# Optimization experiments

Measured on AMD Instinct MI355X. Metric: run time of the kernel, lower is better.

Reference implementation:

```python
import jax, jax.numpy as jnp
import numpy as np

B, S, D = 1, 2048, 4096
H, KVH, DH = 32, 8, 128
NEG_INF = jnp.finfo(jnp.float32).min


def rotate_half(x):
    x1, x2 = jnp.split(x, 2, axis=-1)
    return jnp.concatenate([-x2, x1], axis=-1)


def setup_inputs() -> dict:
    key = jax.random.key(0)
    ks = jax.random.split(key, 6)
    hidden_states = jax.random.normal(ks[0], (B, S, D), dtype=jnp.float32)
    # proper llama RoPE tables
    inv_freq = 1.0 / (10000.0 ** (jnp.arange(0, DH, 2, dtype=jnp.float32) / DH))
    pos = jnp.arange(S, dtype=jnp.float32)
    freqs = pos[:, None] * inv_freq[None, :]            # [S, DH/2]
    emb = jnp.concatenate([freqs, freqs], axis=-1)       # [S, DH]
    cos = jnp.cos(emb)
    sin = jnp.sin(emb)
    # additive causal mask [B,1,S,S]
    causal = jnp.tril(jnp.ones((S, S), dtype=bool))
    attention_mask = jnp.where(causal, 0.0, NEG_INF)[None, None].astype(jnp.float32)
    sc = 0.02
    Wq = jax.random.normal(ks[1], (D, H * DH), dtype=jnp.float32) * sc
    Wk = jax.random.normal(ks[2], (D, KVH * DH), dtype=jnp.float32) * sc
    Wv = jax.random.normal(ks[3], (D, KVH * DH), dtype=jnp.float32) * sc
    Wo = jax.random.normal(ks[4], (H * DH, D), dtype=jnp.float32) * sc
    return {"hidden_states": hidden_states, "cos": cos, "sin": sin,
            "attention_mask": attention_mask, "Wq": Wq, "Wk": Wk, "Wv": Wv, "Wo": Wo}


def reference(hidden_states, cos, sin, attention_mask, Wq, Wk, Wv, Wo):
    b, s, _ = hidden_states.shape
    scaling = DH ** -0.5
    q = (hidden_states @ Wq).reshape(b, s, H, DH).transpose(0, 2, 1, 3)     # [B,H,S,DH]
    k = (hidden_states @ Wk).reshape(b, s, KVH, DH).transpose(0, 2, 1, 3)   # [B,KVH,S,DH]
    v = (hidden_states @ Wv).reshape(b, s, KVH, DH).transpose(0, 2, 1, 3)
    c = cos[None, None]  # [1,1,S,DH]
    sn = sin[None, None]
    q = q * c + rotate_half(q) * sn
    k = k * c + rotate_half(k) * sn
    n_rep = H // KVH
    k = jnp.repeat(k, n_rep, axis=1)  # [B,H,S,DH]
    v = jnp.repeat(v, n_rep, axis=1)
    scores = jnp.einsum('bhqd,bhkd->bhqk', q, k) * scaling
    scores = jnp.maximum(scores + attention_mask, NEG_INF)
    probs = jax.nn.softmax(scores.astype(jnp.float32), axis=-1).astype(q.dtype)
    attn = jnp.einsum('bhqk,bhkd->bhqd', probs, v)
    attn = attn.transpose(0, 2, 1, 3).reshape(b, s, H * DH)
    return attn @ Wo
```

## Files before the change

kernel.cpp:

```cpp
#include <hip/hip_runtime.h>
#include <hip/hip_bf16.h>
#include <stdint.h>

typedef unsigned short u16;
typedef unsigned int u32;
typedef __bf16 bf16x8 __attribute__((ext_vector_type(8)));
typedef float f32x4 __attribute__((ext_vector_type(4)));
typedef u16 u16x8 __attribute__((ext_vector_type(8)));

#define S_LEN 2048
#define DMODEL 4096
#define NHEADS 32
#define NKVH 8
#define DHEAD 128
#define LDQK 6144

__device__ __forceinline__ float bf2f(u16 x) {
    union { u32 i; float f; } u; u.i = ((u32)x) << 16; return u.f;
}
__device__ __forceinline__ u16 f2bf(float f) {
    union { float f; u32 i; } u; u.f = f;
    u32 x = u.i;
    return (u16)((x + 0x7fffu + ((x >> 16) & 1u)) >> 16);
}
__device__ __forceinline__ bf16x8 ld_bf8(const void* p) {
    int4 v = *(const int4*)p;
    return __builtin_bit_cast(bf16x8, v);
}

__global__ void k_cvt(const float* __restrict__ in, u16* __restrict__ out, int n8) {
    int i = blockIdx.x * 256 + threadIdx.x;
    if (i >= n8) return;
    const float4* p = (const float4*)in + (size_t)i * 2;
    float4 a = p[0], b = p[1];
    u16x8 o;
    o[0]=f2bf(a.x); o[1]=f2bf(a.y); o[2]=f2bf(a.z); o[3]=f2bf(a.w);
    o[4]=f2bf(b.x); o[5]=f2bf(b.y); o[6]=f2bf(b.z); o[7]=f2bf(b.w);
    *((u16x8*)out + i) = o;
}

template<typename TIN>
__global__ void k_transpose_bf16(const TIN* __restrict__ in, u16* __restrict__ out,
                                 int R, int C, int ldin) {
    __shared__ u16 tile[32][33];
    int c0 = blockIdx.x * 32, r0 = blockIdx.y * 32;
    int tx = threadIdx.x & 31, ty = threadIdx.x >> 5;
    #pragma unroll
    for (int i = 0; i < 4; i++) {
        int r = ty + i * 8;
        TIN v = in[(size_t)(r0 + r) * ldin + c0 + tx];
        if constexpr (sizeof(TIN) == 4) tile[r][tx] = f2bf((float)v);
        else tile[r][tx] = (u16)v;
    }
    __syncthreads();
    #pragma unroll
    for (int i = 0; i < 4; i++) {
        int r = ty + i * 8;
        out[(size_t)(c0 + r) * R + r0 + tx] = tile[tx][r];
    }
}

__global__ void k_rope(u16* __restrict__ X, const float* __restrict__ cosT,
                       const float* __restrict__ sinT, int nh, int ld) {
    int idx = blockIdx.x * 256 + threadIdx.x;
    int d = idx & 63;
    int h = (idx >> 6) % nh;
    int s = idx / (64 * nh);
    u16* p = X + (size_t)s * ld + h * DHEAD;
    float x1 = bf2f(p[d]), x2 = bf2f(p[d + 64]);
    float c1 = cosT[s * DHEAD + d],      s1 = sinT[s * DHEAD + d];
    float c2 = cosT[s * DHEAD + d + 64], s2 = sinT[s * DHEAD + d + 64];
    p[d]      = f2bf(x1 * c1 - x2 * s1);
    p[d + 64] = f2bf(x2 * c2 + x1 * s2);
}

typedef const __attribute__((address_space(1))) u32 GBUF;
typedef __attribute__((address_space(3))) u32 LBUF;

template<typename OUT_T>
__global__ __launch_bounds__(256)
void k_gemm_bt(const u16* __restrict__ A, const u16* __restrict__ Bt,
               OUT_T* __restrict__ C, int M, int N, int K) {
    __shared__ __align__(16) u16 As[128 * 32];
    __shared__ __align__(16) u16 Bs[128 * 32];
    const int m0 = blockIdx.y * 128, n0 = blockIdx.x * 128;
    const int tid = threadIdx.x, lane = tid & 63, wid = tid >> 6;
    const int wr = wid >> 1, wc = wid & 1;
    const int g = lane >> 4, lr = lane & 15;

    f32x4 acc[4][4] = {};

    for (int k0 = 0; k0 < K; k0 += 32) {
        __syncthreads();
        #pragma unroll
        for (int j = 0; j < 2; j++) {
            int c = wid * 128 + j * 64 + lane;
            int r = c >> 2, co = (c & 3) << 3;
            __builtin_amdgcn_global_load_lds((GBUF*)(A  + (size_t)(m0 + r) * K + k0 + co),
                                             (LBUF*)(As + (size_t)(wid * 128 + j * 64) * 8), 16, 0, 0);
            __builtin_amdgcn_global_load_lds((GBUF*)(Bt + (size_t)(n0 + r) * K + k0 + co),
                                             (LBUF*)(Bs + (size_t)(wid * 128 + j * 64) * 8), 16, 0, 0);
        }
        __syncthreads();
        bf16x8 af[4], bf[4];
        #pragma unroll
        for (int i = 0; i < 4; i++)
            af[i] = ld_bf8(As + (wr * 64 + i * 16 + lr) * 32 + g * 8);
        #pragma unroll
        for (int i = 0; i < 4; i++)
            bf[i] = ld_bf8(Bs + (wc * 64 + i * 16 + lr) * 32 + g * 8);
        #pragma unroll
        for (int i = 0; i < 4; i++)
            #pragma unroll
            for (int n = 0; n < 4; n++)
                acc[i][n] = __builtin_amdgcn_mfma_f32_16x16x32_bf16(af[i], bf[n], acc[i][n], 0, 0, 0);
    }
    #pragma unroll
    for (int i = 0; i < 4; i++)
        #pragma unroll
        for (int n = 0; n < 4; n++)
            #pragma unroll
            for (int r = 0; r < 4; r++) {
                int row = m0 + wr * 64 + i * 16 + g * 4 + r;
                int col = n0 + wc * 64 + n * 16 + lr;
                float v = acc[i][n][r];
                if constexpr (sizeof(OUT_T) == 2) C[(size_t)row * N + col] = f2bf(v);
                else                              C[(size_t)row * N + col] = v;
            }
}

__global__ __launch_bounds__(256)
void k_attn2(const u16* __restrict__ Qb, const u16* __restrict__ Kb,
             const u16* __restrict__ VbT, u16* __restrict__ Ab) {
    extern __shared__ __align__(16) char smem[];

    const int p = blockIdx.x, h = blockIdx.y, hk = h >> 2;
    const int tid = threadIdx.x, lane = tid & 63, wid = tid >> 6;
    const int g = lane >> 4, lr = lane & 15;
    const float scale = 0.08838834764831845f;
    const int qtA = p, qtB = 31 - p, nA = qtA + 1;
    const int NIT = 33;

    const int krow_l = lane >> 4, kc16 = lane & 15;
    const int vrow_l = lane >> 3, vc8  = lane & 7;

    u16* PsB = (u16*)(smem + 65536) + wid * 16 * 72;

    auto stage = [&](int buf, int k0) {
        u16* KsD = (u16*)smem + buf * 8192;
        u16* VtD = (u16*)(smem + 32768) + buf * 8192;
        #pragma unroll
        for (int j = 0; j < 4; j++) {
            int rowt = wid * 16 + j * 4 + krow_l;
            int c16  = kc16 ^ (rowt & 7);
            __builtin_amdgcn_global_load_lds(
                (GBUF*)(Kb + (size_t)(k0 + rowt) * LDQK + hk * DHEAD + c16 * 8),
                (LBUF*)(KsD + (wid * 16 + j * 4) * 128), 16, 0, 0);
        }
        #pragma unroll
        for (int j = 0; j < 4; j++) {
            int rowt = wid * 32 + j * 8 + vrow_l;
            int c8   = vc8 ^ (rowt & 7);
            __builtin_amdgcn_global_load_lds(
                (GBUF*)(VbT + (size_t)(hk * DHEAD + rowt) * S_LEN + k0 + c8 * 8),
                (LBUF*)(VtD + (wid * 32 + j * 8) * 64), 16, 0, 0);
        }
    };

    bf16x8 qf[4];
    f32x4 acc[8];
    float m[4], lsum[4];
    int qt = qtA, q0 = qtA * 64;

    stage(0, 0);
    asm volatile("s_waitcnt vmcnt(0)" ::: "memory");
    __builtin_amdgcn_s_barrier();

    for (int i = 0; i < NIT; i++) {
        const int kt = (i < nA) ? i : (i - nA);
        if (i + 1 < NIT) {
            int kt1 = (i + 1 < nA) ? (i + 1) : (i + 1 - nA);
            stage((i + 1) & 1, kt1 * 64);
        }
        if (i == 0 || i == nA) {
            if (i == nA) {
                #pragma unroll
                for (int n = 0; n < 8; n++)
                    #pragma unroll
                    for (int r = 0; r < 4; r++)
                        Ab[(size_t)(q0 + wid * 16 + g * 4 + r) * DMODEL + h * DHEAD + n * 16 + lr]
                            = f2bf(acc[n][r] / lsum[r]);
            }
            qt = (i == 0) ? qtA : qtB;
            q0 = qt * 64;
            const u16* qrow = Qb + (size_t)(q0 + wid * 16 + lr) * LDQK + h * DHEAD;
            #pragma unroll
            for (int c = 0; c < 4; c++) qf[c] = ld_bf8(qrow + c * 32 + g * 8);
            #pragma unroll
            for (int n = 0; n < 8; n++) acc[n] = (f32x4){0.f, 0.f, 0.f, 0.f};
            #pragma unroll
            for (int r = 0; r < 4; r++) { m[r] = -1e30f; lsum[r] = 0.f; }
        }

        const char* KsB = smem + (i & 1) * 16384;
        const char* VtB = smem + 32768 + (i & 1) * 16384;

        f32x4 sf[4];
        __builtin_amdgcn_s_setprio(1);
        #pragma unroll
        for (int st = 0; st < 4; st++) {
            f32x4 s = {0.f, 0.f, 0.f, 0.f};
            #pragma unroll
            for (int c = 0; c < 4; c++) {
                int row = st * 16 + lr;
                int cb = (c * 32 + g * 8) * 2;
                bf16x8 kf = ld_bf8(KsB + row * 256 + (cb ^ ((row & 7) << 4)));
                s = __builtin_amdgcn_mfma_f32_16x16x32_bf16(qf[c], kf, s, 0, 0, 0);
            }
            sf[st] = s;
        }
        __builtin_amdgcn_s_setprio(0);

        if (kt == qt) {
            #pragma unroll
            for (int st = 0; st < 4; st++)
                #pragma unroll
                for (int r = 0; r < 4; r++) {
                    int qg = wid * 16 + g * 4 + r;
                    int kg = st * 16 + lr;
                    sf[st][r] = (kg > qg) ? -1e30f : sf[st][r] * scale;
                }
        } else {
            #pragma unroll
            for (int st = 0; st < 4; st++)
                #pragma unroll
                for (int r = 0; r < 4; r++) sf[st][r] *= scale;
        }

        float corr[4];
        #pragma unroll
        for (int r = 0; r < 4; r++) {
            float v = fmaxf(fmaxf(sf[0][r], sf[1][r]), fmaxf(sf[2][r], sf[3][r]));
            #pragma unroll
            for (int off = 1; off < 16; off <<= 1) v = fmaxf(v, __shfl_xor(v, off, 64));
            float mn = fmaxf(m[r], v);
            corr[r] = __expf(m[r] - mn);
            m[r] = mn;
        }
        float ts[4] = {0.f, 0.f, 0.f, 0.f};
        #pragma unroll
        for (int st = 0; st < 4; st++)
            #pragma unroll
            for (int r = 0; r < 4; r++) {
                float pv = __expf(sf[st][r] - m[r]);
                sf[st][r] = pv;
                ts[r] += pv;
            }
        #pragma unroll
        for (int r = 0; r < 4; r++) {
            #pragma unroll
            for (int off = 1; off < 16; off <<= 1) ts[r] += __shfl_xor(ts[r], off, 64);
            lsum[r] = lsum[r] * corr[r] + ts[r];
        }
        #pragma unroll
        for (int n = 0; n < 8; n++)
            #pragma unroll
            for (int r = 0; r < 4; r++) acc[n][r] *= corr[r];

        #pragma unroll
        for (int st = 0; st < 4; st++)
            #pragma unroll
            for (int r = 0; r < 4; r++)
                PsB[(g * 4 + r) * 72 + st * 16 + lr] = f2bf(sf[st][r]);
        asm volatile("s_waitcnt lgkmcnt(0)" ::: "memory");

        __builtin_amdgcn_s_setprio(1);
        #pragma unroll
        for (int c2 = 0; c2 < 2; c2++) {
            bf16x8 pa = ld_bf8(PsB + lr * 72 + c2 * 32 + g * 8);
            #pragma unroll
            for (int n = 0; n < 8; n++) {
                int row = n * 16 + lr;
                int cb = (c2 * 32 + g * 8) * 2;
                bf16x8 vf = ld_bf8(VtB + row * 128 + (cb ^ ((row & 7) << 4)));
                acc[n] = __builtin_amdgcn_mfma_f32_16x16x32_bf16(pa, vf, acc[n], 0, 0, 0);
            }
        }
        __builtin_amdgcn_s_setprio(0);

        asm volatile("s_waitcnt lgkmcnt(0)" ::: "memory");
        __builtin_amdgcn_sched_barrier(0);
        asm volatile("s_waitcnt vmcnt(0)" ::: "memory");
        __builtin_amdgcn_s_barrier();
    }

    #pragma unroll
    for (int n = 0; n < 8; n++)
        #pragma unroll
        for (int r = 0; r < 4; r++)
            Ab[(size_t)(q0 + wid * 16 + g * 4 + r) * DMODEL + h * DHEAD + n * 16 + lr]
                = f2bf(acc[n][r] / lsum[r]);
}

extern "C" void kernel_launch(void* const* d_in, const int* in_sizes, int n_in,
                              void* d_out, int out_size, void* d_ws, size_t ws_size,
                              hipStream_t stream) {
    const float* hidden = (const float*)d_in[0];
    const float* cosT   = (const float*)d_in[1];
    const float* sinT   = (const float*)d_in[2];
    const float* Wq = (const float*)d_in[4];
    const float* Wk = (const float*)d_in[5];
    const float* Wv = (const float*)d_in[6];
    const float* Wo = (const float*)d_in[7];
    float* out = (float*)d_out;
    char* ws = (char*)d_ws;

    u16* Xbf   = (u16*)ws;
    u16* WqkvT = (u16*)(ws + (16u << 20));
    u16* VbT   = (u16*)(ws + (16u << 20));
    u16* WoT   = (u16*)(ws + (64u << 20));
    u16* QKVb  = (u16*)(ws + (96u << 20));
    u16* Ab    = Xbf;

    k_cvt<<<dim3((S_LEN * DMODEL / 8) / 256), 256, 0, stream>>>(hidden, Xbf, S_LEN * DMODEL / 8);
    k_transpose_bf16<float><<<dim3(4096 / 32, 4096 / 32), 256, 0, stream>>>(Wq, WqkvT, 4096, 4096, 4096);
    k_transpose_bf16<float><<<dim3(1024 / 32, 4096 / 32), 256, 0, stream>>>(Wk, WqkvT + (size_t)4096 * 4096, 4096, 1024, 1024);
    k_transpose_bf16<float><<<dim3(1024 / 32, 4096 / 32), 256, 0, stream>>>(Wv, WqkvT + (size_t)5120 * 4096, 4096, 1024, 1024);
    k_transpose_bf16<float><<<dim3(4096 / 32, 4096 / 32), 256, 0, stream>>>(Wo, WoT, 4096, 4096, 4096);

    k_gemm_bt<u16><<<dim3(6144 / 128, 2048 / 128), 256, 0, stream>>>(Xbf, WqkvT, QKVb, 2048, 6144, 4096);

    k_rope<<<(2048 * 32 * 64) / 256, 256, 0, stream>>>(QKVb, cosT, sinT, 32, LDQK);
    k_rope<<<(2048 * 8 * 64) / 256, 256, 0, stream>>>(QKVb + 4096, cosT, sinT, 8, LDQK);

    k_transpose_bf16<u16><<<dim3(1024 / 32, 2048 / 32), 256, 0, stream>>>(QKVb + 5120, VbT, 2048, 1024, LDQK);

    hipFuncSetAttribute((const void*)k_attn2, hipFuncAttributeMaxDynamicSharedMemorySize, 74752);
    k_attn2<<<dim3(16, 32), 256, 74752, stream>>>(QKVb, QKVb + 4096, VbT, Ab);

    k_gemm_bt<float><<<dim3(4096 / 128, 2048 / 128), 256, 0, stream>>>(Ab, WoT, out, 2048, 4096, 4096);
}
```

Measured before the change: 411.6 us.

## Replace 128x128 GEMM with pipelined 256x256 tile kernel and split-K output projection

Replaces the simple 128x128-tile GEMM with a 512-thread 256x256-tile kernel. It double-buffers 64-wide K slices in 128KB of LDS with XOR-swizzled layout, interleaves async global->LDS loads with MFMA phases, and uses setprio and an XCD-aware block swizzle. The QKV projection runs 192 tiles. The output projection uses split-K by 2 into a scratch buffer plus the output, then adds them in an extra kernel. This should raise arithmetic intensity and overlap loads with compute, at the cost of an extra fp32 read-modify-write pass and heavier register and LDS use.

Result: slower. 511.6 us (+24.3%).

```diff
diff --git a/kernel.cpp b/kernel.cpp
--- a/kernel.cpp
+++ b/kernel.cpp
@@ -78,55 +78,136 @@
 typedef __attribute__((address_space(3))) u32 LBUF;
 
 template<typename OUT_T>
-__global__ __launch_bounds__(256)
-void k_gemm_bt(const u16* __restrict__ A, const u16* __restrict__ Bt,
-               OUT_T* __restrict__ C, int M, int N, int K) {
-    __shared__ __align__(16) u16 As[128 * 32];
-    __shared__ __align__(16) u16 Bs[128 * 32];
-    const int m0 = blockIdx.y * 128, n0 = blockIdx.x * 128;
+__global__ __launch_bounds__(512, 2)
+void k_gemm256(const u16* __restrict__ A, const u16* __restrict__ Bt,
+               OUT_T* __restrict__ C0, OUT_T* __restrict__ C1,
+               int M, int N, int K, int mtiles, int ntiles, int k_len) {
+    extern __shared__ __align__(16) char smem[];
+
+    const int nwg = gridDim.x;
+    const int cpx = nwg >> 3;
+    const int flat = blockIdx.x;
+    const int swz = (flat & 7) * cpx + (flat >> 3);
+    const int tile = swz % (mtiles * ntiles);
+    const int kz = swz / (mtiles * ntiles);
+    const int bm = (tile / ntiles) * 256, bn = (tile % ntiles) * 256;
+    const int k0b = kz * k_len;
+    OUT_T* __restrict__ Cz = kz ? C1 : C0;
+
     const int tid = threadIdx.x, lane = tid & 63, wid = tid >> 6;
-    const int wr = wid >> 1, wc = wid & 1;
+    const int wr = wid >> 2, wc = wid & 3;
     const int g = lane >> 4, lr = lane & 15;
-
-    f32x4 acc[4][4] = {};
-
-    for (int k0 = 0; k0 < K; k0 += 32) {
-        __syncthreads();
+    const u32 lrsw = ((lr >> 2) & 1) << 5;
+
+    const u16* srcA[2]; const u16* srcB[2]; u32 ldsl[2];
+    #pragma unroll
+    for (int j = 0; j < 2; j++) {
+        int c = j * 512 + tid;
+        int rowc = c >> 3;
+        int colsw = (c & 7) ^ (((c >> 5) & 1) << 1);
+        srcA[j] = A  + (size_t)(bm + rowc) * K + k0b + colsw * 8;
+        srcB[j] = Bt + (size_t)(bn + rowc) * K + k0b + colsw * 8;
+        ldsl[j] = (u32)(j * 512 + wid * 64) * 16;
+    }
+
+    auto stageHT = [&](int buf, int kind, int half, int kt) {
         #pragma unroll
         for (int j = 0; j < 2; j++) {
-            int c = wid * 128 + j * 64 + lane;
-            int r = c >> 2, co = (c & 3) << 3;
-            __builtin_amdgcn_global_load_lds((GBUF*)(A  + (size_t)(m0 + r) * K + k0 + co),
-                                             (LBUF*)(As + (size_t)(wid * 128 + j * 64) * 8), 16, 0, 0);
-            __builtin_amdgcn_global_load_lds((GBUF*)(Bt + (size_t)(n0 + r) * K + k0 + co),
-                                             (LBUF*)(Bs + (size_t)(wid * 128 + j * 64) * 8), 16, 0, 0);
-        }
-        __syncthreads();
-        bf16x8 af[4], bf[4];
-        #pragma unroll
-        for (int i = 0; i < 4; i++)
-            af[i] = ld_bf8(As + (wr * 64 + i * 16 + lr) * 32 + g * 8);
-        #pragma unroll
-        for (int i = 0; i < 4; i++)
-            bf[i] = ld_bf8(Bs + (wc * 64 + i * 16 + lr) * 32 + g * 8);
-        #pragma unroll
-        for (int i = 0; i < 4; i++)
-            #pragma unroll
-            for (int n = 0; n < 4; n++)
-                acc[i][n] = __builtin_amdgcn_mfma_f32_16x16x32_bf16(af[i], bf[n], acc[i][n], 0, 0, 0);
+            const u16* src = (kind ? srcB[j] : srcA[j]) + (size_t)half * 128 * K + kt * 64;
+            u32 off = (u32)kind * 65536 + (u32)buf * 32768 + (u32)half * 16384 + ldsl[j];
+            __builtin_amdgcn_global_load_lds((GBUF*)src, (LBUF*)(smem + off), 16, 0, 0);
+        }
+    };
+
+    f32x4 acc[8][4] = {};
+    bf16x8 af[4][2], bfr[2][2];
+
+    const int NT = k_len >> 6;
+
+    stageHT(0, 0, 0, 0); stageHT(0, 0, 1, 0); stageHT(0, 1, 0, 0); stageHT(0, 1, 1, 0);
+    stageHT(1, 0, 0, 1);
+    __builtin_amdgcn_sched_barrier(0);
+    asm volatile("s_waitcnt vmcnt(2)" ::: "memory");
+    __builtin_amdgcn_sched_barrier(0);
+    __builtin_amdgcn_s_barrier();
+
+    const int stg_buf[8] = {1,1,1, 0,0,0,0, 1};
+    const int stg_ht [8] = {1,2,3, 0,1,2,3, 0};
+
+    for (int t = 0; t < (NT >> 1); t++) {
+        const int kt1 = 2 * t + 1;
+        int kt2 = 2 * t + 2; if (kt2 >= NT) kt2 -= NT;
+        int kt3 = 2 * t + 3; if (kt3 >= NT) kt3 -= NT;
+        #pragma unroll
+        for (int p = 0; p < 8; p++) {
+            const int q = p & 3, bs = p >> 2;
+            const int mh = q & 1, nh = q >> 1;
+            if (p != 3 && p != 7) {
+                int kts = (p < 3) ? kt1 : kt2;
+                stageHT(stg_buf[p], stg_ht[p] >> 1, stg_ht[p] & 1, kts);
+            }
+            if ((q & 1) == 0) {
+                #pragma unroll
+                for (int n2 = 0; n2 < 2; n2++)
+                    #pragma unroll
+                    for (int kk = 0; kk < 2; kk++)
+                        bfr[n2][kk] = ld_bf8(smem + 65536 + bs * 32768 + (wc >> 1) * 16384 +
+                            ((u32)(((wc & 1) * 64 + (nh * 2 + n2) * 16 + lr) * 128 + kk * 64 + g * 16) ^ lrsw));
+            }
+            #pragma unroll
+            for (int m4 = 0; m4 < 4; m4++)
+                #pragma unroll
+                for (int kk = 0; kk < 2; kk++)
+                    af[m4][kk] = ld_bf8(smem + bs * 32768 + wr * 16384 +
+                        ((u32)(((mh * 4 + m4) * 16 + lr) * 128 + kk * 64 + g * 16) ^ lrsw));
+            __builtin_amdgcn_sched_barrier(0);
+            __builtin_amdgcn_s_barrier();
+            asm volatile("s_waitcnt lgkmcnt(0)" ::: "memory");
+            __builtin_amdgcn_sched_barrier(0);
+            __builtin_amdgcn_s_setprio(1);
+            #pragma unroll
+            for (int m4 = 0; m4 < 4; m4++)
+                #pragma unroll
+                for (int n2 = 0; n2 < 2; n2++)
+                    #pragma unroll
+                    for (int kk = 0; kk < 2; kk++)
+                        acc[mh * 4 + m4][nh * 2 + n2] = __builtin_amdgcn_mfma_f32_16x16x32_bf16(
+                            af[m4][kk], bfr[n2][kk], acc[mh * 4 + m4][nh * 2 + n2], 0, 0, 0);
+            __builtin_amdgcn_s_setprio(0);
+            if (p == 3 || p == 7) {
+                int kts = (p == 3) ? kt2 : kt3;
+                stageHT(stg_buf[p], stg_ht[p] >> 1, stg_ht[p] & 1, kts);
+                __builtin_amdgcn_sched_barrier(0);
+                asm volatile("s_waitcnt vmcnt(2)" ::: "memory");
+                __builtin_amdgcn_sched_barrier(0);
+            }
+            __builtin_amdgcn_s_barrier();
+        }
     }
+
     #pragma unroll
-    for (int i = 0; i < 4; i++)
+    for (int m = 0; m < 8; m++)
         #pragma unroll
         for (int n = 0; n < 4; n++)
             #pragma unroll
             for (int r = 0; r < 4; r++) {
-                int row = m0 + wr * 64 + i * 16 + g * 4 + r;
-                int col = n0 + wc * 64 + n * 16 + lr;
-                float v = acc[i][n][r];
-                if constexpr (sizeof(OUT_T) == 2) C[(size_t)row * N + col] = f2bf(v);
-                else                              C[(size_t)row * N + col] = v;
-            }
+                int row = bm + wr * 128 + m * 16 + g * 4 + r;
+                int col = bn + wc * 64 + n * 16 + lr;
+                float v = acc[m][n][r];
+                if constexpr (sizeof(OUT_T) == 2) Cz[(size_t)row * N + col] = f2bf(v);
+                else                              Cz[(size_t)row * N + col] = v;
+            }
+}
+
+__global__ void k_addp(const float* __restrict__ p0, float* __restrict__ out, int n8) {
+    int i = blockIdx.x * 256 + threadIdx.x;
+    if (i >= n8) return;
+    const float4* a = (const float4*)p0 + (size_t)i * 2;
+    float4* o = (float4*)out + (size_t)i * 2;
+    float4 a0 = a[0], a1 = a[1], o0 = o[0], o1 = o[1];
+    o0.x += a0.x; o0.y += a0.y; o0.z += a0.z; o0.w += a0.w;
+    o1.x += a1.x; o1.y += a1.y; o1.z += a1.z; o1.w += a1.w;
+    o[0] = o0; o[1] = o1;
 }
 
 __global__ __launch_bounds__(256)
@@ -315,12 +396,13 @@
     float* out = (float*)d_out;
     char* ws = (char*)d_ws;
 
-    u16* Xbf   = (u16*)ws;
-    u16* WqkvT = (u16*)(ws + (16u << 20));
-    u16* VbT   = (u16*)(ws + (16u << 20));
-    u16* WoT   = (u16*)(ws + (64u << 20));
-    u16* QKVb  = (u16*)(ws + (96u << 20));
-    u16* Ab    = Xbf;
+    u16*   Xbf   = (u16*)ws;
+    u16*   WqkvT = (u16*)(ws + (16u << 20));
+    u16*   VbT   = (u16*)(ws + (16u << 20));
+    float* P0    = (float*)(ws + (20u << 20));
+    u16*   WoT   = (u16*)(ws + (64u << 20));
+    u16*   QKVb  = (u16*)(ws + (96u << 20));
+    u16*   Ab    = Xbf;
 
     k_cvt<<<dim3((S_LEN * DMODEL / 8) / 256), 256, 0, stream>>>(hidden, Xbf, S_LEN * DMODEL / 8);
     k_transpose_bf16<float><<<dim3(4096 / 32, 4096 / 32), 256, 0, stream>>>(Wq, WqkvT, 4096, 4096, 4096);
@@ -328,7 +410,10 @@
     k_transpose_bf16<float><<<dim3(1024 / 32, 4096 / 32), 256, 0, stream>>>(Wv, WqkvT + (size_t)5120 * 4096, 4096, 1024, 1024);
     k_transpose_bf16<float><<<dim3(4096 / 32, 4096 / 32), 256, 0, stream>>>(Wo, WoT, 4096, 4096, 4096);
 
-    k_gemm_bt<u16><<<dim3(6144 / 128, 2048 / 128), 256, 0, stream>>>(Xbf, WqkvT, QKVb, 2048, 6144, 4096);
+    hipFuncSetAttribute((const void*)k_gemm256<u16>,  hipFuncAttributeMaxDynamicSharedMemorySize, 131072);
+    hipFuncSetAttribute((const void*)k_gemm256<float>, hipFuncAttributeMaxDynamicSharedMemorySize, 131072);
+
+    k_gemm256<u16><<<192, 512, 131072, stream>>>(Xbf, WqkvT, QKVb, QKVb, 2048, 6144, 4096, 8, 24, 4096);
 
     k_rope<<<(2048 * 32 * 64) / 256, 256, 0, stream>>>(QKVb, cosT, sinT, 32, LDQK);
     k_rope<<<(2048 * 8 * 64) / 256, 256, 0, stream>>>(QKVb + 4096, cosT, sinT, 8, LDQK);
@@ -338,5 +423,6 @@
     hipFuncSetAttribute((const void*)k_attn2, hipFuncAttributeMaxDynamicSharedMemorySize, 74752);
     k_attn2<<<dim3(16, 32), 256, 74752, stream>>>(QKVb, QKVb + 4096, VbT, Ab);
 
-    k_gemm_bt<float><<<dim3(4096 / 128, 2048 / 128), 256, 0, stream>>>(Ab, WoT, out, 2048, 4096, 4096);
-}
+    k_gemm256<float><<<256, 512, 131072, stream>>>(Ab, WoT, P0, out, 2048, 4096, 4096, 8, 16, 2048);
+    k_addp<<<(2048 * 4096 / 8) / 256, 256, 0, stream>>>(P0, out, 2048 * 4096 / 8);
+}
```

## Deepen GEMM K-tile to 64 with swizzled LDS and add lazy softmax rescaling

Applied to the files above, without the earlier changes.

The GEMM kernel now loads a 64-wide K slice per iteration into an XOR-swizzled shared-memory layout. This halves the number of barrier pairs per K loop and is meant to avoid LDS bank conflicts on fragment reads, at the cost of doubling LDS use per block. In attention, the running max is only updated when a new tile's max exceeds it by more than 8. When no row in the wave needs an update, the accumulator rescale is skipped, which trades a bounded risk of exp growth for fewer multiplies.

New measurement: 372.5 us. 9.5% less time.

```diff
diff --git a/kernel.cpp b/kernel.cpp
--- a/kernel.cpp
+++ b/kernel.cpp
@@ -79,41 +79,60 @@
 
 template<typename OUT_T>
 __global__ __launch_bounds__(256)
-void k_gemm_bt(const u16* __restrict__ A, const u16* __restrict__ Bt,
-               OUT_T* __restrict__ C, int M, int N, int K) {
-    __shared__ __align__(16) u16 As[128 * 32];
-    __shared__ __align__(16) u16 Bs[128 * 32];
+void k_gemm_bt2(const u16* __restrict__ A, const u16* __restrict__ Bt,
+                OUT_T* __restrict__ C, int M, int N, int K) {
+    __shared__ __align__(16) u16 As[128 * 64];
+    __shared__ __align__(16) u16 Bs[128 * 64];
     const int m0 = blockIdx.y * 128, n0 = blockIdx.x * 128;
     const int tid = threadIdx.x, lane = tid & 63, wid = tid >> 6;
     const int wr = wid >> 1, wc = wid & 1;
     const int g = lane >> 4, lr = lane & 15;
 
+    const u16* sA[4]; const u16* sB[4]; u32 dste[4];
+    #pragma unroll
+    for (int j = 0; j < 4; j++) {
+        int c = j * 256 + tid;
+        int row = c >> 3;
+        int colsw = (c & 7) ^ (row & 7);
+        sA[j] = A  + (size_t)(m0 + row) * K + colsw * 8;
+        sB[j] = Bt + (size_t)(n0 + row) * K + colsw * 8;
+        dste[j] = (u32)c * 8;
+    }
+    auto rdoff = [&](int row, int kk) -> u32 {
+        return (u32)(row * 128 + ((((kk << 2) + g) ^ (row & 7)) << 4));
+    };
+
     f32x4 acc[4][4] = {};
 
-    for (int k0 = 0; k0 < K; k0 += 32) {
+    for (int k0 = 0; k0 < K; k0 += 64) {
         __syncthreads();
         #pragma unroll
-        for (int j = 0; j < 2; j++) {
-            int c = wid * 128 + j * 64 + lane;
-            int r = c >> 2, co = (c & 3) << 3;
-            __builtin_amdgcn_global_load_lds((GBUF*)(A  + (size_t)(m0 + r) * K + k0 + co),
-                                             (LBUF*)(As + (size_t)(wid * 128 + j * 64) * 8), 16, 0, 0);
-            __builtin_amdgcn_global_load_lds((GBUF*)(Bt + (size_t)(n0 + r) * K + k0 + co),
-                                             (LBUF*)(Bs + (size_t)(wid * 128 + j * 64) * 8), 16, 0, 0);
-        }
+        for (int j = 0; j < 4; j++)
+            __builtin_amdgcn_global_load_lds((GBUF*)(sA[j] + k0), (LBUF*)(As + dste[j]), 16, 0, 0);
+        #pragma unroll
+        for (int j = 0; j < 4; j++)
+            __builtin_amdgcn_global_load_lds((GBUF*)(sB[j] + k0), (LBUF*)(Bs + dste[j]), 16, 0, 0);
         __syncthreads();
-        bf16x8 af[4], bf[4];
+
+        bf16x8 af[4][2], bfv[4][2];
         #pragma unroll
         for (int i = 0; i < 4; i++)
-            af[i] = ld_bf8(As + (wr * 64 + i * 16 + lr) * 32 + g * 8);
+            #pragma unroll
+            for (int kk = 0; kk < 2; kk++)
+                af[i][kk] = ld_bf8((const char*)As + rdoff(wr * 64 + i * 16 + lr, kk));
+        #pragma unroll
+        for (int n = 0; n < 4; n++)
+            #pragma unroll
+            for (int kk = 0; kk < 2; kk++)
+                bfv[n][kk] = ld_bf8((const char*)Bs + rdoff(wc * 64 + n * 16 + lr, kk));
         #pragma unroll
         for (int i = 0; i < 4; i++)
-            bf[i] = ld_bf8(Bs + (wc * 64 + i * 16 + lr) * 32 + g * 8);
-        #pragma unroll
-        for (int i = 0; i < 4; i++)
             #pragma unroll
             for (int n = 0; n < 4; n++)
-                acc[i][n] = __builtin_amdgcn_mfma_f32_16x16x32_bf16(af[i], bf[n], acc[i][n], 0, 0, 0);
+                #pragma unroll
+                for (int kk = 0; kk < 2; kk++)
+                    acc[i][n] = __builtin_amdgcn_mfma_f32_16x16x32_bf16(
+                        af[i][kk], bfv[n][kk], acc[i][n], 0, 0, 0);
     }
     #pragma unroll
     for (int i = 0; i < 4; i++)
@@ -238,14 +257,17 @@
         }
 
         float corr[4];
+        int allskip = 1;
         #pragma unroll
         for (int r = 0; r < 4; r++) {
             float v = fmaxf(fmaxf(sf[0][r], sf[1][r]), fmaxf(sf[2][r], sf[3][r]));
             #pragma unroll
             for (int off = 1; off < 16; off <<= 1) v = fmaxf(v, __shfl_xor(v, off, 64));
-            float mn = fmaxf(m[r], v);
-            corr[r] = __expf(m[r] - mn);
+            bool sk = (v <= m[r] + 8.0f);
+            float mn = sk ? m[r] : v;
+            corr[r] = sk ? 1.0f : __expf(m[r] - mn);
             m[r] = mn;
+            allskip &= (int)sk;
         }
         float ts[4] = {0.f, 0.f, 0.f, 0.f};
         #pragma unroll
@@ -262,10 +284,12 @@
             for (int off = 1; off < 16; off <<= 1) ts[r] += __shfl_xor(ts[r], off, 64);
             lsum[r] = lsum[r] * corr[r] + ts[r];
         }
-        #pragma unroll
-        for (int n = 0; n < 8; n++)
-            #pragma unroll
-            for (int r = 0; r < 4; r++) acc[n][r] *= corr[r];
+        if (!__all(allskip)) {
+            #pragma unroll
+            for (int n = 0; n < 8; n++)
+                #pragma unroll
+                for (int r = 0; r < 4; r++) acc[n][r] *= corr[r];
+        }
 
         #pragma unroll
         for (int st = 0; st < 4; st++)
@@ -328,7 +352,7 @@
     k_transpose_bf16<float><<<dim3(1024 / 32, 4096 / 32), 256, 0, stream>>>(Wv, WqkvT + (size_t)5120 * 4096, 4096, 1024, 1024);
     k_transpose_bf16<float><<<dim3(4096 / 32, 4096 / 32), 256, 0, stream>>>(Wo, WoT, 4096, 4096, 4096);
 
-    k_gemm_bt<u16><<<dim3(6144 / 128, 2048 / 128), 256, 0, stream>>>(Xbf, WqkvT, QKVb, 2048, 6144, 4096);
+    k_gemm_bt2<u16><<<dim3(6144 / 128, 2048 / 128), 256, 0, stream>>>(Xbf, WqkvT, QKVb, 2048, 6144, 4096);
 
     k_rope<<<(2048 * 32 * 64) / 256, 256, 0, stream>>>(QKVb, cosT, sinT, 32, LDQK);
     k_rope<<<(2048 * 8 * 64) / 256, 256, 0, stream>>>(QKVb + 4096, cosT, sinT, 8, LDQK);
@@ -338,5 +362,5 @@
     hipFuncSetAttribute((const void*)k_attn2, hipFuncAttributeMaxDynamicSharedMemorySize, 74752);
     k_attn2<<<dim3(16, 32), 256, 74752, stream>>>(QKVb, QKVb + 4096, VbT, Ab);
 
-    k_gemm_bt<float><<<dim3(4096 / 128, 2048 / 128), 256, 0, stream>>>(Ab, WoT, out, 2048, 4096, 4096);
-}
+    k_gemm_bt2<float><<<dim3(4096 / 128, 2048 / 128), 256, 0, stream>>>(Ab, WoT, out, 2048, 4096, 4096);
+}
```
